# Kernel tuning notes

Hardware: AMD Instinct MI355X
Metric: run time of the kernel (lower is better)

Reference implementation:

```python
import jax, jax.numpy as jnp
import numpy as np

N_MODELS = 64
IN_F = 256
OUT_F = 256
BATCH = 8192


def setup_inputs() -> dict:
    key = jax.random.key(0)
    kx, kw, kb, ki = jax.random.split(key, 4)
    x = jax.random.normal(kx, (BATCH, OUT_F), dtype=jnp.float32)
    idxs = jax.random.randint(ki, (BATCH,), 0, N_MODELS, dtype=jnp.int64)
    # learned parameters (torch inits them to zeros; we use random so grads/outputs are nontrivial)
    w = jax.random.normal(kw, (N_MODELS, IN_F, OUT_F), dtype=jnp.float32) * 0.02
    b = jax.random.normal(kb, (N_MODELS, OUT_F), dtype=jnp.float32) * 0.02
    return {"x": x, "idxs": idxs, "w": w, "b": b}


def reference(x, idxs, w, b):
    # torch: baddbmm(b[idxs,:,None], w[idxs], x[:,:,None]).squeeze(-1) -> relu
    # y[n, i] = b[idxs[n], i] + sum_o w[idxs[n], i, o] * x[n, o]
    wg = w[idxs]                      # (B, in, out) gathered per-sample weights
    bg = b[idxs]                      # (B, out)
    y = jnp.einsum('bio,bo->bi', wg, x) + bg
    return jax.nn.relu(y)
```

## Files before the change

kernel.cpp:

```cpp
#include <hip/hip_runtime.h>
#include <stdint.h>


#define N_MODELS 64
#define IN_F     256
#define OUT_F    256
#define BATCH    8192
#define BM       128
#define BN       128
#define PKX      264

typedef __bf16 bf16x8 __attribute__((ext_vector_type(8)));
typedef float  f32x4  __attribute__((ext_vector_type(4)));
typedef __attribute__((address_space(3))) uint32_t lds_u32;
typedef const __attribute__((address_space(1))) uint32_t glb_u32;

__device__ __forceinline__ void dma16(const void* g, void* l) {
  __builtin_amdgcn_global_load_lds((glb_u32*)g, (lds_u32*)l, 16, 0, 0);
}

__device__ __forceinline__ void barrier_lds_only() {
  asm volatile("s_waitcnt lgkmcnt(0)" ::: "memory");
  __builtin_amdgcn_s_barrier();
  __builtin_amdgcn_sched_barrier(0);
}

__device__ __forceinline__ bf16x8 pack8(float4 a, float4 b) {
  bf16x8 o;
  o[0] = (__bf16)a.x; o[1] = (__bf16)a.y; o[2] = (__bf16)a.z; o[3] = (__bf16)a.w;
  o[4] = (__bf16)b.x; o[5] = (__bf16)b.y; o[6] = (__bf16)b.z; o[7] = (__bf16)b.w;
  return o;
}

__global__ __launch_bounds__(1024) void fused_kernel(
    const float* __restrict__ x, const int* __restrict__ idxs,
    const float* __restrict__ w, const float* __restrict__ bias_g,
    float* __restrict__ out) {
  const int b     = (blockIdx.x & 7) * 32 + (blockIdx.x >> 3);
  const int model = b >> 2;
  const int s     = (b >> 1) & 1;
  const int i0    = (b & 1) * BN;
  const int t     = threadIdx.x;
  const int lane  = t & 63;
  const int wv    = t >> 6;

  __shared__ float w_lds[2][BM][64];
  __shared__ unsigned short a_lds[BM][PKX];
  __shared__ int rid[BM];
  __shared__ int wsum[16];

  const int4* ip = (const int4*)idxs + t * 2;
  int4 iv0 = ip[0], iv1 = ip[1];

  const float* wbase = w + (size_t)model * (IN_F * OUT_F) + (size_t)i0 * IN_F;
  const int l_r = lane >> 4;
  const int l_c = lane & 15;
#define W_DMA(q, buf)                                                        \
  {                                                                          \
    _Pragma("unroll")                                                        \
    for (int j = 0; j < 2; ++j) {                                            \
      const int r0 = wv * 8 + j * 4;                                         \
      const int rr = r0 + l_r;                                               \
      const float* gs = wbase + (size_t)rr * IN_F + (q) * 64                 \
                        + ((l_c ^ (rr & 7)) << 2);                           \
      dma16(gs, &w_lds[buf][r0][0]);                                         \
    }                                                                        \
  }

  if (s == 0) { W_DMA(0, 0) W_DMA(1, 1) }

  if (t < BM) rid[t] = -1;

  int cnt = (iv0.x == model) + (iv0.y == model) + (iv0.z == model) + (iv0.w == model)
          + (iv1.x == model) + (iv1.y == model) + (iv1.z == model) + (iv1.w == model);
  int inc = cnt;
#pragma unroll
  for (int d = 1; d < 64; d <<= 1) {
    int u = __shfl_up(inc, d);
    if (lane >= d) inc += u;
  }
  if (lane == 63) wsum[wv] = inc;
  barrier_lds_only();
  int wpre = 0, total = 0;
#pragma unroll
  for (int j = 0; j < 16; ++j) {
    int sj = wsum[j];
    total += sj;
    if (j < wv) wpre += sj;
  }
  const int start = s * BM;
  if (start >= total) return;
  if (s == 1) { W_DMA(0, 0) W_DMA(1, 1) }

  int off = wpre + inc - cnt - start;
  {
    int n0 = t * 8;
    if (iv0.x == model) { if ((unsigned)off < BM) rid[off] = n0 + 0; ++off; }
    if (iv0.y == model) { if ((unsigned)off < BM) rid[off] = n0 + 1; ++off; }
    if (iv0.z == model) { if ((unsigned)off < BM) rid[off] = n0 + 2; ++off; }
    if (iv0.w == model) { if ((unsigned)off < BM) rid[off] = n0 + 3; ++off; }
    if (iv1.x == model) { if ((unsigned)off < BM) rid[off] = n0 + 4; ++off; }
    if (iv1.y == model) { if ((unsigned)off < BM) rid[off] = n0 + 5; ++off; }
    if (iv1.z == model) { if ((unsigned)off < BM) rid[off] = n0 + 6; ++off; }
    if (iv1.w == model) { if ((unsigned)off < BM) rid[off] = n0 + 7; ++off; }
  }
  barrier_lds_only();

  const int rwx = t >> 3;
  const int hx  = t & 7;
  const int srow = rid[rwx];
  const float* xrow = x + (size_t)(srow < 0 ? 0 : srow) * IN_F + hx * 32;
  {
    float4 tx[8];
#pragma unroll
    for (int j = 0; j < 8; ++j) tx[j] = *(const float4*)(xrow + j * 4);
#pragma unroll
    for (int j = 0; j < 4; ++j)
      *(bf16x8*)&a_lds[rwx][hx * 32 + j * 8] = pack8(tx[2 * j], tx[2 * j + 1]);
  }

  const int wm   = (wv & 3) * 32;
  const int wn   = (wv >> 2) * 32;
  const int col  = lane & 15;
  const int quad = lane >> 4;
  float bv[2];
  const float* bp = bias_g + model * OUT_F + i0 + wn + col;
#pragma unroll
  for (int nt = 0; nt < 2; ++nt) bv[nt] = bp[nt * 16];

  __syncthreads();

  f32x4 acc[2][2];
#pragma unroll
  for (int mt = 0; mt < 2; ++mt)
#pragma unroll
    for (int nt = 0; nt < 2; ++nt)
      acc[mt][nt] = (f32x4){bv[nt], bv[nt], bv[nt], bv[nt]};

#define MFMA_QUARTER(buf, ks0)                                               \
  {                                                                          \
    _Pragma("unroll")                                                        \
    for (int kk = 0; kk < 2; ++kk) {                                         \
      const int ks  = (ks0) + kk;                                            \
      const int ch0 = kk * 8 + quad * 2;                                     \
      bf16x8 af[2], bfr[2];                                                  \
      _Pragma("unroll")                                                      \
      for (int mt = 0; mt < 2; ++mt)                                         \
        af[mt] = *(const bf16x8*)&a_lds[wm + mt * 16 + col]                  \
                                      [ks * 32 + quad * 8];                  \
      _Pragma("unroll")                                                      \
      for (int nt = 0; nt < 2; ++nt) {                                       \
        const int R  = wn + nt * 16 + col;                                   \
        const int sw = R & 7;                                                \
        float4 f0 = *(const float4*)&w_lds[buf][R][((ch0)     ^ sw) << 2];   \
        float4 f1 = *(const float4*)&w_lds[buf][R][((ch0 + 1) ^ sw) << 2];   \
        bfr[nt] = pack8(f0, f1);                                             \
      }                                                                      \
      _Pragma("unroll")                                                      \
      for (int mt = 0; mt < 2; ++mt)                                         \
        _Pragma("unroll")                                                    \
        for (int nt = 0; nt < 2; ++nt)                                       \
          acc[mt][nt] = __builtin_amdgcn_mfma_f32_16x16x32_bf16(             \
              af[mt], bfr[nt], acc[mt][nt], 0, 0, 0);                        \
    }                                                                        \
  }

  MFMA_QUARTER(0, 0)
  __syncthreads();
  W_DMA(2, 0)
  MFMA_QUARTER(1, 2)
  __syncthreads();
  W_DMA(3, 1)
  MFMA_QUARTER(0, 4)
  __syncthreads();
  MFMA_QUARTER(1, 6)

#pragma unroll
  for (int mt = 0; mt < 2; ++mt) {
#pragma unroll
    for (int reg = 0; reg < 4; ++reg) {
      const int mm = wm + mt * 16 + quad * 4 + reg;
      const int sle = rid[mm];
      if (sle >= 0) {
        float* orow = out + (size_t)sle * OUT_F + i0 + wn + col;
#pragma unroll
        for (int nt = 0; nt < 2; ++nt)
          orow[nt * 16] = fmaxf(acc[mt][nt][reg], 0.0f);
      }
    }
  }
#undef W_DMA
#undef MFMA_QUARTER
}

extern "C" void kernel_launch(void* const* d_in, const int* in_sizes, int n_in,
                              void* d_out, int out_size, void* d_ws, size_t ws_size,
                              hipStream_t stream) {
  const float* x    = (const float*)d_in[0];
  const int*   idxs = (const int*)d_in[1];
  const float* w    = (const float*)d_in[2];
  const float* b    = (const float*)d_in[3];
  float* out = (float*)d_out;
  (void)d_ws; (void)ws_size;

  fused_kernel<<<N_MODELS * 4, 1024, 0, stream>>>(x, idxs, w, b, out);
}
```

Measured before the change: 86.20 us.

## Stream gathered x rows via async LDS DMA, double-buffered with weights

```diff
diff --git a/kernel.cpp b/kernel.cpp
--- a/kernel.cpp
+++ b/kernel.cpp
@@ -8,7 +8,6 @@
 #define BATCH    8192
 #define BM       128
 #define BN       128
-#define PKX      264
 
 typedef __bf16 bf16x8 __attribute__((ext_vector_type(8)));
 typedef float  f32x4  __attribute__((ext_vector_type(4)));
@@ -45,12 +44,9 @@
   const int wv    = t >> 6;
 
   __shared__ float w_lds[2][BM][64];
-  __shared__ unsigned short a_lds[BM][PKX];
+  __shared__ float x_lds[2][BM][64];
   __shared__ int rid[BM];
   __shared__ int wsum[16];
-
-  const int4* ip = (const int4*)idxs + t * 2;
-  int4 iv0 = ip[0], iv1 = ip[1];
 
   const float* wbase = w + (size_t)model * (IN_F * OUT_F) + (size_t)i0 * IN_F;
   const int l_r = lane >> 4;
@@ -67,6 +63,9 @@
     }                                                                        \
   }
 
+  const int4* ip = (const int4*)idxs + t * 2;
+  int4 iv0 = ip[0], iv1 = ip[1];
+
   if (s == 0) { W_DMA(0, 0) W_DMA(1, 1) }
 
   if (t < BM) rid[t] = -1;
@@ -106,18 +105,22 @@
   }
   barrier_lds_only();
 
-  const int rwx = t >> 3;
-  const int hx  = t & 7;
-  const int srow = rid[rwx];
-  const float* xrow = x + (size_t)(srow < 0 ? 0 : srow) * IN_F + hx * 32;
-  {
-    float4 tx[8];
-#pragma unroll
-    for (int j = 0; j < 8; ++j) tx[j] = *(const float4*)(xrow + j * 4);
-#pragma unroll
-    for (int j = 0; j < 4; ++j)
-      *(bf16x8*)&a_lds[rwx][hx * 32 + j * 8] = pack8(tx[2 * j], tx[2 * j + 1]);
-  }
+  const int   r_0 = wv * 4 + l_r;
+  const int   r_1 = 64 + wv * 4 + l_r;
+  const int   sr0 = rid[r_0];
+  const int   sr1 = rid[r_1];
+  const float* xb0 = x + (size_t)(sr0 < 0 ? 0 : sr0) * IN_F
+                       + ((l_c ^ (r_0 & 7)) << 2);
+  const float* xb1 = x + (size_t)(sr1 < 0 ? 0 : sr1) * IN_F
+                       + ((l_c ^ (r_1 & 7)) << 2);
+#define X_DMA(q, buf)                                                        \
+  {                                                                          \
+    dma16(xb0 + (q) * 64, &x_lds[buf][wv * 4][0]);                           \
+    dma16(xb1 + (q) * 64, &x_lds[buf][64 + wv * 4][0]);                      \
+  }
+
+  X_DMA(0, 0)
+  X_DMA(1, 1)
 
   const int wm   = (wv & 3) * 32;
   const int wn   = (wv >> 2) * 32;
@@ -141,13 +144,16 @@
   {                                                                          \
     _Pragma("unroll")                                                        \
     for (int kk = 0; kk < 2; ++kk) {                                         \
-      const int ks  = (ks0) + kk;                                            \
       const int ch0 = kk * 8 + quad * 2;                                     \
       bf16x8 af[2], bfr[2];                                                  \
       _Pragma("unroll")                                                      \
-      for (int mt = 0; mt < 2; ++mt)                                         \
-        af[mt] = *(const bf16x8*)&a_lds[wm + mt * 16 + col]                  \
-                                      [ks * 32 + quad * 8];                  \
+      for (int mt = 0; mt < 2; ++mt) {                                       \
+        const int Ra  = wm + mt * 16 + col;                                  \
+        const int swa = Ra & 7;                                              \
+        float4 a0 = *(const float4*)&x_lds[buf][Ra][((ch0)     ^ swa) << 2]; \
+        float4 a1 = *(const float4*)&x_lds[buf][Ra][((ch0 + 1) ^ swa) << 2]; \
+        af[mt] = pack8(a0, a1);                                              \
+      }                                                                      \
       _Pragma("unroll")                                                      \
       for (int nt = 0; nt < 2; ++nt) {                                       \
         const int R  = wn + nt * 16 + col;                                   \
@@ -167,10 +173,10 @@
 
   MFMA_QUARTER(0, 0)
   __syncthreads();
-  W_DMA(2, 0)
+  W_DMA(2, 0) X_DMA(2, 0)
   MFMA_QUARTER(1, 2)
   __syncthreads();
-  W_DMA(3, 1)
+  W_DMA(3, 1) X_DMA(3, 1)
   MFMA_QUARTER(0, 4)
   __syncthreads();
   MFMA_QUARTER(1, 6)
@@ -190,6 +196,7 @@
     }
   }
 #undef W_DMA
+#undef X_DMA
 #undef MFMA_QUARTER
 }
 
```

Result: faster. 83.70 us (median of 2 runs) (-2.9%).
